# Kernel tuning notes

Measured on AMD Instinct MI355X. Metric: run time of the kernel, lower is better.

The kernel has to match this reference:

```python
import jax, jax.numpy as jnp
import numpy as np
import math

K = 3
IN_CH = 512
OUT_CH = 512
W_DIM = 512
B = 16
HW = 64
LR_MUL = 1.0


def setup_inputs() -> dict:
    key = jax.random.key(0)
    k1, k2, k3, k4 = jax.random.split(key, 4)
    x = jax.random.normal(k1, (B, HW, HW, IN_CH), dtype=jnp.float32)
    w_latents = jax.random.normal(k2, (B, W_DIM), dtype=jnp.float32)
    w = jax.random.normal(k3, (K, K, IN_CH, OUT_CH), dtype=jnp.float32)  # init_std = 1/lr_mul = 1
    b = jnp.zeros((OUT_CH,), dtype=jnp.float32)
    fc_w = jax.random.normal(k4, (W_DIM, IN_CH), dtype=jnp.float32)
    fc_b = jnp.zeros((IN_CH,), dtype=jnp.float32)
    return {"x": x, "w_latents": w_latents, "w": w, "b": b, "fc_w": fc_w, "fc_b": fc_b}


def reference(x, w_latents, w, b, fc_w, fc_b):
    # equalized-LR runtime coefficients (gain=1)
    conv_coef = LR_MUL / math.sqrt(K * K * IN_CH)
    fc_coef = LR_MUL / math.sqrt(W_DIM)

    batch, H, W_, Cin = x.shape
    x_nchw = jnp.transpose(x, (0, 3, 1, 2))  # [B, Cin, H, W]

    weight = w * conv_coef  # [k,k,in,out]
    # style modulation: fully_connected (no lrelu) + 1
    s = w_latents @ (fc_w * fc_coef) + fc_b * LR_MUL + 1.0  # [B, in]

    # per-sample modulated weights [B,k,k,in,out]
    ww = weight[None] * s[:, None, None, :, None]
    # demodulation
    d = jax.lax.rsqrt(jnp.sum(jnp.square(ww), axis=(1, 2, 3)) + 1e-8)  # [B, out]
    ww = ww * d[:, None, None, None, :]

    # fused_modconv: grouped conv with groups = batch
    x_g = x_nchw.reshape(1, batch * Cin, H, W_)
    w_g = jnp.transpose(ww, (1, 2, 3, 0, 4)).reshape(K, K, Cin, batch * OUT_CH)
    y = jax.lax.conv_general_dilated(
        x_g, w_g,
        window_strides=(1, 1),
        padding='SAME',
        dimension_numbers=('NCHW', 'HWIO', 'NCHW'),
        feature_group_count=batch,
    )  # [1, B*out, H, W]
    y = y.reshape(batch, OUT_CH, H, W_)
    y = jnp.transpose(y, (0, 2, 3, 1))  # NHWC
    y = y + (b * LR_MUL)
    return y
```

## Files before the change

### kernel.cpp

```cpp
#include <hip/hip_runtime.h>
#include <hip/hip_bf16.h>

#define IN_CH 512
#define OUT_CH 512
#define W_DIM 512
#define BATCH 16
#define HWDIM 64
#define PADW 66

static constexpr float CONV_COEF = 0.014731391274719739f;
static constexpr float FC_COEF   = 0.044194173824159216f;

typedef __bf16 bf16x8 __attribute__((ext_vector_type(8)));
typedef float  f32x4  __attribute__((ext_vector_type(4)));

typedef __attribute__((address_space(1))) void gvoid;
typedef __attribute__((address_space(3))) void lvoid;

__device__ __forceinline__ void async_cp16(const void* g, void* l) {
    __builtin_amdgcn_global_load_lds((gvoid*)g, (lvoid*)l, 16, 0, 0);
}

__device__ __forceinline__ ushort f2bf(float f) {
    union { float f; unsigned u; } un; un.f = f;
    unsigned u = un.u;
    return (ushort)((u + 0x7fffu + ((u >> 16) & 1u)) >> 16);
}

__global__ void k_halo(ushort* __restrict__ xs) {
    int b = blockIdx.y;
    int pidx = blockIdx.x * 4 + (threadIdx.x >> 6);
    int ch = threadIdx.x & 63;
    int h, w;
    if (pidx < 66)       { h = 0;          w = pidx; }
    else if (pidx < 132) { h = 65;         w = pidx - 66; }
    else if (pidx < 196) { h = pidx - 131; w = 0; }
    else                 { h = pidx - 195; w = 65; }
    size_t base = (((size_t)(b * PADW + h)) * PADW + w) * IN_CH + ch * 8;
    uint4 z = {0u, 0u, 0u, 0u};
    *(uint4*)(xs + base) = z;
}

__global__ void k_style(const float* __restrict__ wl, const float* __restrict__ fcw,
                        const float* __restrict__ fcb, float* __restrict__ s) {
    int b = blockIdx.x;
    int i = blockIdx.y * 128 + threadIdx.x;
    __shared__ float lw[W_DIM];
    for (int j = threadIdx.x; j < W_DIM; j += 128) lw[j] = wl[b * W_DIM + j];
    __syncthreads();
    float acc = 0.f;
#pragma unroll 8
    for (int j = 0; j < W_DIM; ++j) acc += lw[j] * fcw[(size_t)j * IN_CH + i];
    s[b * IN_CH + i] = acc * FC_COEF + fcb[i] + 1.0f;
}

__global__ void k_xs(const float* __restrict__ x, const float* __restrict__ s,
                     ushort* __restrict__ xs) {
    int t = blockIdx.x * blockDim.x + threadIdx.x;
    int pix = t >> 7;
    int c = (t & 127) << 2;
    int b = pix >> 12;
    int hw = pix & 4095;
    int h = hw >> 6, w = hw & 63;
    float4 xv = ((const float4*)x)[t];
    float4 sv = ((const float4*)(s + b * IN_CH))[t & 127];
    ushort4 o;
    o.x = f2bf(xv.x * sv.x);
    o.y = f2bf(xv.y * sv.y);
    o.z = f2bf(xv.z * sv.z);
    o.w = f2bf(xv.w * sv.w);
    size_t dst = (((size_t)(b * PADW + h + 1)) * PADW + (w + 1)) * IN_CH + c;
    *(ushort4*)(xs + dst) = o;
}

__global__ void k_wt(const float* __restrict__ w, ushort* __restrict__ wT) {
    __shared__ float tile[32][33];
    int kk = blockIdx.z;
    const float* src = w + (size_t)kk * IN_CH * OUT_CH;
    ushort* dst = wT + (size_t)kk * IN_CH * OUT_CH;
    int i0 = blockIdx.y * 32;
    int o0 = blockIdx.x * 32;
    int tx = threadIdx.x, ty = threadIdx.y;
#pragma unroll
    for (int rr = 0; rr < 32; rr += 8)
        tile[ty + rr][tx] = src[(size_t)(i0 + ty + rr) * OUT_CH + o0 + tx];
    __syncthreads();
#pragma unroll
    for (int rr = 0; rr < 32; rr += 8)
        dst[(size_t)(o0 + ty + rr) * IN_CH + i0 + tx] = f2bf(tile[tx][ty + rr]);
}

__global__ void k_a2(const float* __restrict__ w, float* __restrict__ a2) {
    int n = blockIdx.x * blockDim.x + threadIdx.x;
    float sum = 0.f;
#pragma unroll
    for (int kk = 0; kk < 9; ++kk) {
        float v = w[(size_t)kk * (IN_CH * OUT_CH) + n];
        sum += v * v;
    }
    a2[n] = sum;
}

__global__ void k_dmod(const float* __restrict__ s, const float* __restrict__ a2,
                       float* __restrict__ dmod) {
    int b = blockIdx.x;
    int o = blockIdx.y * 128 + threadIdx.x;
    __shared__ float s2[IN_CH];
    for (int i = threadIdx.x; i < IN_CH; i += 128) {
        float v = s[b * IN_CH + i];
        s2[i] = v * v;
    }
    __syncthreads();
    float acc = 0.f;
#pragma unroll 8
    for (int i = 0; i < IN_CH; ++i) acc += s2[i] * a2[(size_t)i * OUT_CH + o];
    dmod[b * OUT_CH + o] = rsqrtf(acc * CONV_COEF * CONV_COEF + 1e-8f);
}

__global__ __launch_bounds__(256) void k_conv(
    const ushort* __restrict__ xs, const ushort* __restrict__ wT,
    const float* __restrict__ dmod, const float* __restrict__ bias,
    float* __restrict__ out) {
    __shared__ ushort sA[128 * 64];
    __shared__ ushort sB[128 * 64];

    const int tid = threadIdx.x;
    const int wave = tid >> 6;
    const int lane = tid & 63;

    const int bid = blockIdx.x;
    const int mt = (bid & 7) | ((bid >> 5) << 3);
    const int nt = (bid >> 3) & 3;
    const int b  = mt >> 5;
    const int h0 = (mt & 31) << 1;
    const int n0 = nt << 7;

    const int srow = tid >> 3;
    const int lc   = (tid & 7) ^ (srow & 7);

    const ushort* gA[4];
    const ushort* gB[4];
#pragma unroll
    for (int i = 0; i < 4; ++i) {
        int row = i * 32 + srow;
        int rh  = row >> 6;
        int w   = row & 63;
        gA[i] = xs + (((size_t)(b * PADW + h0 + rh)) * PADW + w) * IN_CH + lc * 8;
        gB[i] = wT + ((size_t)(n0 + row)) * IN_CH + lc * 8;
    }
    ushort* dA[4];
    ushort* dB[4];
#pragma unroll
    for (int i = 0; i < 4; ++i) {
        dA[i] = sA + (i * 256 + wave * 64) * 8;
        dB[i] = sB + (i * 256 + wave * 64) * 8;
    }

    const int r = lane & 15;
    const int q = lane >> 4;
    const int wr = (wave & 1) << 6;
    const int wc = (wave >> 1) << 6;

    const ushort* aRd[2][4];
    const ushort* bRd[2][4];
#pragma unroll
    for (int ks = 0; ks < 2; ++ks)
#pragma unroll
        for (int f = 0; f < 4; ++f) {
            int rowA = wr + f * 16 + r;
            aRd[ks][f] = sA + rowA * 64 + ((ks * 4 + q) ^ (rowA & 7)) * 8;
            int rowB = wc + f * 16 + r;
            bRd[ks][f] = sB + rowB * 64 + ((ks * 4 + q) ^ (rowB & 7)) * 8;
        }

    f32x4 acc[4][4];
#pragma unroll
    for (int i = 0; i < 4; ++i)
#pragma unroll
        for (int j = 0; j < 4; ++j) {
            f32x4 z = {0.f, 0.f, 0.f, 0.f};
            acc[i][j] = z;
        }

    for (int kk = 0; kk < 9; ++kk) {
        const int aoff = ((kk / 3) * PADW + (kk % 3)) * IN_CH;
        const size_t boff = (size_t)kk * (IN_CH * OUT_CH);
        for (int c0 = 0; c0 < IN_CH; c0 += 64) {
            __syncthreads();
#pragma unroll
            for (int i = 0; i < 4; ++i) {
                async_cp16(gA[i] + aoff + c0, dA[i]);
                async_cp16(gB[i] + boff + c0, dB[i]);
            }
            __syncthreads();
#pragma unroll
            for (int ks = 0; ks < 2; ++ks) {
                bf16x8 av[4], bv[4];
#pragma unroll
                for (int f = 0; f < 4; ++f) av[f] = *(const bf16x8*)aRd[ks][f];
#pragma unroll
                for (int f = 0; f < 4; ++f) bv[f] = *(const bf16x8*)bRd[ks][f];
#pragma unroll
                for (int i = 0; i < 4; ++i)
#pragma unroll
                    for (int j = 0; j < 4; ++j)
                        acc[i][j] = __builtin_amdgcn_mfma_f32_16x16x32_bf16(
                            av[i], bv[j], acc[i][j], 0, 0, 0);
            }
        }
    }

#pragma unroll
    for (int j = 0; j < 4; ++j) {
        const int n = n0 + wc + j * 16 + r;
        const float scale = dmod[b * OUT_CH + n] * CONV_COEF;
        const float bv2 = bias[n];
#pragma unroll
        for (int i = 0; i < 4; ++i) {
#pragma unroll
            for (int e = 0; e < 4; ++e) {
                const int m = wr + i * 16 + q * 4 + e;
                const int h = h0 + (m >> 6);
                const int w = m & 63;
                out[(((size_t)(b * HWDIM + h)) * HWDIM + w) * OUT_CH + n] =
                    acc[i][j][e] * scale + bv2;
            }
        }
    }
}

extern "C" void kernel_launch(void* const* d_in, const int* in_sizes, int n_in,
                              void* d_out, int out_size, void* d_ws, size_t ws_size,
                              hipStream_t stream) {
    const float* x    = (const float*)d_in[0];
    const float* wl   = (const float*)d_in[1];
    const float* w    = (const float*)d_in[2];
    const float* bias = (const float*)d_in[3];
    const float* fcw  = (const float*)d_in[4];
    const float* fcb  = (const float*)d_in[5];
    float* out = (float*)d_out;

    char* ws = (char*)d_ws;
    const size_t XS_BYTES = (size_t)BATCH * PADW * PADW * IN_CH * 2;
    const size_t WT_BYTES = (size_t)9 * IN_CH * OUT_CH * 2;
    ushort* xs   = (ushort*)ws;
    ushort* wT   = (ushort*)(ws + XS_BYTES);
    float*  s    = (float*)(ws + XS_BYTES + WT_BYTES);
    float*  dmod = s + BATCH * IN_CH;
    float*  a2   = dmod + BATCH * OUT_CH;

    k_halo<<<dim3(65, BATCH), 256, 0, stream>>>(xs);
    k_style<<<dim3(BATCH, 4), 128, 0, stream>>>(wl, fcw, fcb, s);
    k_xs<<<(BATCH * HWDIM * HWDIM * IN_CH / 4) / 256, 256, 0, stream>>>(x, s, xs);
    k_wt<<<dim3(16, 16, 9), dim3(32, 8), 0, stream>>>(w, wT);
    k_a2<<<(IN_CH * OUT_CH) / 256, 256, 0, stream>>>(w, a2);
    k_dmod<<<dim3(BATCH, 4), 128, 0, stream>>>(s, a2, dmod);
    k_conv<<<2048, 256, 0, stream>>>(xs, wT, dmod, bias, out);
}
```

Measured before the change: 576.5 us.

## Enlarge conv tiles to 256x256 with double-buffered async LDS pipeline

The implicit-GEMM conv kernel now uses 512-thread blocks computing 256x256 output tiles (8 waves, each 128x64) instead of 128x128, raising data reuse per LDS load. Global-to-LDS async copies are double-buffered, so the next K-slice streams in while MFMAs run on the current one, with explicit vmcnt waits and barriers. It also adds s_setprio around the MFMA bursts and remaps blocks so each XCD works on a contiguous group of tiles. The costs are higher register pressure (128 accumulator floats per lane), 128KB of LDS per block, and fewer blocks (512) on the device.

```diff
diff --git a/kernel.cpp b/kernel.cpp
--- a/kernel.cpp
+++ b/kernel.cpp
@@ -117,109 +117,147 @@
     dmod[b * OUT_CH + o] = rsqrtf(acc * CONV_COEF * CONV_COEF + 1e-8f);
 }
 
-__global__ __launch_bounds__(256) void k_conv(
+
+__device__ __forceinline__ int aoff_of(int t) {
+    int kk = t >> 3;
+    int c0 = (t & 7) << 6;
+    int kh = (kk >= 6) ? 2 : ((kk >= 3) ? 1 : 0);
+    int kw = kk - kh * 3;
+    return (kh * PADW + kw) * IN_CH + c0;
+}
+
+__device__ __forceinline__ int boff_of(int t) {
+    int kk = t >> 3;
+    int c0 = (t & 7) << 6;
+    return kk * (IN_CH * OUT_CH) + c0;
+}
+
+__device__ __forceinline__ void stage8(const ushort* gA, const ushort* gB,
+                                       ushort* dA, ushort* dB) {
+#pragma unroll
+    for (int i = 0; i < 4; ++i) {
+        async_cp16(gA + i * (PADW * IN_CH), dA + i * 4096);
+        async_cp16(gB + i * (64 * IN_CH), dB + i * 4096);
+    }
+}
+
+__device__ __forceinline__ void compute_step(
+        const ushort* aB0, const ushort* aB1,
+        const ushort* bB0, const ushort* bB1,
+        f32x4 (&acc)[8][4]) {
+#pragma unroll
+    for (int ks = 0; ks < 2; ++ks) {
+        const ushort* aB = ks ? aB1 : aB0;
+        const ushort* bB = ks ? bB1 : bB0;
+        bf16x8 bv[4];
+#pragma unroll
+        for (int j = 0; j < 4; ++j) bv[j] = *(const bf16x8*)(bB + j * 1024);
+#pragma unroll
+        for (int mh = 0; mh < 2; ++mh) {
+            bf16x8 av[4];
+#pragma unroll
+            for (int f = 0; f < 4; ++f)
+                av[f] = *(const bf16x8*)(aB + (mh * 4 + f) * 1024);
+            __builtin_amdgcn_s_setprio(1);
+#pragma unroll
+            for (int i = 0; i < 4; ++i)
+#pragma unroll
+                for (int j = 0; j < 4; ++j)
+                    acc[mh * 4 + i][j] = __builtin_amdgcn_mfma_f32_16x16x32_bf16(
+                        av[i], bv[j], acc[mh * 4 + i][j], 0, 0, 0);
+            __builtin_amdgcn_s_setprio(0);
+        }
+    }
+}
+
+__global__ __launch_bounds__(512, 2) void k_conv(
     const ushort* __restrict__ xs, const ushort* __restrict__ wT,
     const float* __restrict__ dmod, const float* __restrict__ bias,
     float* __restrict__ out) {
-    __shared__ ushort sA[128 * 64];
-    __shared__ ushort sB[128 * 64];
+    __shared__ __align__(16) ushort smem[4][16384];
 
     const int tid = threadIdx.x;
     const int wave = tid >> 6;
     const int lane = tid & 63;
-
-    const int bid = blockIdx.x;
-    const int mt = (bid & 7) | ((bid >> 5) << 3);
-    const int nt = (bid >> 3) & 3;
-    const int b  = mt >> 5;
-    const int h0 = (mt & 31) << 1;
-    const int n0 = nt << 7;
-
     const int srow = tid >> 3;
-    const int lc   = (tid & 7) ^ (srow & 7);
-
-    const ushort* gA[4];
-    const ushort* gB[4];
-#pragma unroll
-    for (int i = 0; i < 4; ++i) {
-        int row = i * 32 + srow;
-        int rh  = row >> 6;
-        int w   = row & 63;
-        gA[i] = xs + (((size_t)(b * PADW + h0 + rh)) * PADW + w) * IN_CH + lc * 8;
-        gB[i] = wT + ((size_t)(n0 + row)) * IN_CH + lc * 8;
-    }
-    ushort* dA[4];
-    ushort* dB[4];
-#pragma unroll
-    for (int i = 0; i < 4; ++i) {
-        dA[i] = sA + (i * 256 + wave * 64) * 8;
-        dB[i] = sB + (i * 256 + wave * 64) * 8;
-    }
-
-    const int r = lane & 15;
+    const int lc = (tid & 7) ^ (srow & 7);
+
+    const int wg = (blockIdx.x & 7) * 64 + (blockIdx.x >> 3);
+    const int nt = wg >> 8;
+    const int mt = wg & 255;
+    const int b  = mt >> 4;
+    const int h0 = (mt & 15) << 2;
+    const int n0 = nt << 8;
+
+    const ushort* gA0 = xs + (((size_t)(b * PADW + h0)) * PADW + srow) * IN_CH + lc * 8;
+    const ushort* gB0 = wT + ((size_t)(n0 + srow)) * IN_CH + lc * 8;
+
+    ushort* dA[2] = { &smem[0][wave * 512], &smem[2][wave * 512] };
+    ushort* dB[2] = { &smem[1][wave * 512], &smem[3][wave * 512] };
+
+    const int rlane = lane & 15;
     const int q = lane >> 4;
-    const int wr = (wave & 1) << 6;
-    const int wc = (wave >> 1) << 6;
-
-    const ushort* aRd[2][4];
-    const ushort* bRd[2][4];
-#pragma unroll
-    for (int ks = 0; ks < 2; ++ks)
-#pragma unroll
-        for (int f = 0; f < 4; ++f) {
-            int rowA = wr + f * 16 + r;
-            aRd[ks][f] = sA + rowA * 64 + ((ks * 4 + q) ^ (rowA & 7)) * 8;
-            int rowB = wc + f * 16 + r;
-            bRd[ks][f] = sB + rowB * 64 + ((ks * 4 + q) ^ (rowB & 7)) * 8;
-        }
-
-    f32x4 acc[4][4];
-#pragma unroll
-    for (int i = 0; i < 4; ++i)
+    const int wm = wave >> 2;
+    const int wn = wave & 3;
+    const int pc0 = ((q + 0) ^ (rlane & 7)) * 8;
+    const int pc1 = ((q + 4) ^ (rlane & 7)) * 8;
+
+    const ushort* aR[2][2];
+    const ushort* bR[2][2];
+#pragma unroll
+    for (int bf = 0; bf < 2; ++bf) {
+        aR[bf][0] = &smem[bf * 2][(wm * 128 + rlane) * 64 + pc0];
+        aR[bf][1] = &smem[bf * 2][(wm * 128 + rlane) * 64 + pc1];
+        bR[bf][0] = &smem[bf * 2 + 1][(wn * 64 + rlane) * 64 + pc0];
+        bR[bf][1] = &smem[bf * 2 + 1][(wn * 64 + rlane) * 64 + pc1];
+    }
+
+    f32x4 acc[8][4];
+#pragma unroll
+    for (int i = 0; i < 8; ++i)
 #pragma unroll
         for (int j = 0; j < 4; ++j) {
             f32x4 z = {0.f, 0.f, 0.f, 0.f};
             acc[i][j] = z;
         }
 
-    for (int kk = 0; kk < 9; ++kk) {
-        const int aoff = ((kk / 3) * PADW + (kk % 3)) * IN_CH;
-        const size_t boff = (size_t)kk * (IN_CH * OUT_CH);
-        for (int c0 = 0; c0 < IN_CH; c0 += 64) {
-            __syncthreads();
-#pragma unroll
-            for (int i = 0; i < 4; ++i) {
-                async_cp16(gA[i] + aoff + c0, dA[i]);
-                async_cp16(gB[i] + boff + c0, dB[i]);
-            }
-            __syncthreads();
-#pragma unroll
-            for (int ks = 0; ks < 2; ++ks) {
-                bf16x8 av[4], bv[4];
-#pragma unroll
-                for (int f = 0; f < 4; ++f) av[f] = *(const bf16x8*)aRd[ks][f];
-#pragma unroll
-                for (int f = 0; f < 4; ++f) bv[f] = *(const bf16x8*)bRd[ks][f];
-#pragma unroll
-                for (int i = 0; i < 4; ++i)
-#pragma unroll
-                    for (int j = 0; j < 4; ++j)
-                        acc[i][j] = __builtin_amdgcn_mfma_f32_16x16x32_bf16(
-                            av[i], bv[j], acc[i][j], 0, 0, 0);
-            }
-        }
+    stage8(gA0 + aoff_of(0), gB0 + boff_of(0), dA[0], dB[0]);
+
+#pragma unroll 1
+    for (int t = 0; t < 72; t += 2) {
+        stage8(gA0 + aoff_of(t + 1), gB0 + boff_of(t + 1), dA[1], dB[1]);
+        asm volatile("s_waitcnt vmcnt(8)" ::: "memory");
+        __builtin_amdgcn_s_barrier();
+        asm volatile("" ::: "memory");
+        compute_step(aR[0][0], aR[0][1], bR[0][0], bR[0][1], acc);
+        asm volatile("" ::: "memory");
+        __builtin_amdgcn_s_barrier();
+        asm volatile("" ::: "memory");
+
+        if (t + 2 < 72) {
+            stage8(gA0 + aoff_of(t + 2), gB0 + boff_of(t + 2), dA[0], dB[0]);
+            asm volatile("s_waitcnt vmcnt(8)" ::: "memory");
+        } else {
+            asm volatile("s_waitcnt vmcnt(0)" ::: "memory");
+        }
+        __builtin_amdgcn_s_barrier();
+        asm volatile("" ::: "memory");
+        compute_step(aR[1][0], aR[1][1], bR[1][0], bR[1][1], acc);
+        asm volatile("" ::: "memory");
+        __builtin_amdgcn_s_barrier();
+        asm volatile("" ::: "memory");
     }
 
 #pragma unroll
     for (int j = 0; j < 4; ++j) {
-        const int n = n0 + wc + j * 16 + r;
+        const int n = n0 + wn * 64 + j * 16 + rlane;
         const float scale = dmod[b * OUT_CH + n] * CONV_COEF;
         const float bv2 = bias[n];
 #pragma unroll
-        for (int i = 0; i < 4; ++i) {
+        for (int i = 0; i < 8; ++i) {
 #pragma unroll
             for (int e = 0; e < 4; ++e) {
-                const int m = wr + i * 16 + q * 4 + e;
+                const int m = wm * 128 + i * 16 + q * 4 + e;
                 const int h = h0 + (m >> 6);
                 const int w = m & 63;
                 out[(((size_t)(b * HWDIM + h)) * HWDIM + w) * OUT_CH + n] =
@@ -255,5 +293,5 @@
     k_wt<<<dim3(16, 16, 9), dim3(32, 8), 0, stream>>>(w, wT);
     k_a2<<<(IN_CH * OUT_CH) / 256, 256, 0, stream>>>(w, a2);
     k_dmod<<<dim3(BATCH, 4), 128, 0, stream>>>(s, a2, dmod);
-    k_conv<<<2048, 256, 0, stream>>>(xs, wT, dmod, bias, out);
-}
+    k_conv<<<512, 512, 0, stream>>>(xs, wT, dmod, bias, out);
+}
```

After: 564.2 us. 2.1% less time.
